# Optimization experiments

Measured on AMD Instinct MI355X. Metric: run time of the kernel, lower is better.

The kernel has to match this reference:

```python
import math
import jax, jax.numpy as jnp
import numpy as np

B, T, E = 2, 2048, 2048
H, HKV = 16, 4
DH = E // H              # 128
ROT_DIM = DH             # rotary_pct = 1.0 -> 128
ROT_HALF = ROT_DIM // 2  # RotaryEmbedding is built with dim=ROT_DIM//2=64; only these dims rotate
MAX_SEQ = 2048


def _rope_tables():
    # theta = 10000 ** (-arange(0, dim, 2)/dim) with dim = ROT_HALF
    theta = 10000.0 ** (-jnp.arange(0, ROT_HALF, 2, dtype=jnp.float32) / ROT_HALF)  # [ROT_HALF//2]
    pos = jnp.arange(MAX_SEQ, dtype=jnp.float32)
    angles = pos[:, None] * theta[None, :]   # [MAX_SEQ, ROT_HALF//2]
    return jnp.cos(angles), jnp.sin(angles)


def _apply_rotary(q, k, start_pos):
    # q: [B,T,H,ROT_DIM], k: [B,T,HKV,ROT_DIM]; rotate only first ROT_HALF dims (interleaved pairs)
    cos, sin = _rope_tables()
    t = q.shape[1]
    cos = jax.lax.dynamic_slice_in_dim(cos, start_pos, t, axis=0)[None, :, None, :]
    sin = jax.lax.dynamic_slice_in_dim(sin, start_pos, t, axis=0)[None, :, None, :]

    def rot(a):
        a_rot, a_pass = a[..., :ROT_HALF], a[..., ROT_HALF:]
        x, y = a_rot[..., 0::2], a_rot[..., 1::2]
        rx = x * cos - y * sin
        ry = x * sin + y * cos
        rotated = jnp.stack([rx, ry], axis=-1).reshape(*a_rot.shape)
        return jnp.concatenate([rotated, a_pass], axis=-1)

    return rot(q), rot(k)


def setup_inputs() -> dict:
    key = jax.random.key(0)
    ks = jax.random.split(key, 9)
    s = 0.02  # weight scale for sane logits
    return {
        "x": jax.random.normal(ks[0], (B, T, E), dtype=jnp.float32),
        "Wq": jax.random.normal(ks[1], (E, H * DH), dtype=jnp.float32) * s,
        "bq": jax.random.normal(ks[2], (H * DH,), dtype=jnp.float32) * s,
        "Wk": jax.random.normal(ks[3], (E, HKV * DH), dtype=jnp.float32) * s,
        "bk": jax.random.normal(ks[4], (HKV * DH,), dtype=jnp.float32) * s,
        "Wv": jax.random.normal(ks[5], (E, HKV * DH), dtype=jnp.float32) * s,
        "bv": jax.random.normal(ks[6], (HKV * DH,), dtype=jnp.float32) * s,
        "Wo": jax.random.normal(ks[7], (E, E), dtype=jnp.float32) * s,
        "bo": jax.random.normal(ks[8], (E,), dtype=jnp.float32) * s,
        "start_pos": 0,
    }


def reference(x, Wq, bq, Wk, bk, Wv, bv, Wo, bo, start_pos):
    b, t, _ = x.shape
    q = (x @ Wq + bq).reshape(b, t, H, DH)
    k = (x @ Wk + bk).reshape(b, t, HKV, DH)
    v = (x @ Wv + bv).reshape(b, t, HKV, DH)

    q, k = _apply_rotary(q, k, start_pos)

    group = H // HKV
    k = jnp.repeat(k, group, axis=2)  # [b,t,H,DH]
    v = jnp.repeat(v, group, axis=2)

    # scores: [b,H,t,t]
    scores = jnp.einsum("bqhd,bkhd->bhqk", q, k) / math.sqrt(DH)
    causal = jnp.tril(jnp.ones((t, t), dtype=bool))
    scores = jnp.where(causal[None, None], scores, -jnp.inf)
    probs = jax.nn.softmax(scores, axis=-1)

    out = jnp.einsum("bhqk,bkhd->bqhd", probs, v).reshape(b, t, H * DH)
    return out @ Wo + bo
```

## Files before the change

kernel.cpp:

```cpp
#include <hip/hip_runtime.h>

typedef __attribute__((ext_vector_type(8))) short short8;
typedef __attribute__((ext_vector_type(4))) float f32x4;
typedef __attribute__((ext_vector_type(16))) float f32x16;

#define DEVFN __device__ __forceinline__

DEVFN unsigned short f2bf(float f) {
  unsigned int u = __builtin_bit_cast(unsigned int, f);
  u += 0x7FFFu + ((u >> 16) & 1u);
  return (unsigned short)(u >> 16);
}
DEVFN float bf2f(unsigned int u) { return __builtin_bit_cast(float, u << 16); }

DEVFN unsigned int cvtpk_bf16(float lo, float hi) {
  unsigned int d;
  asm("v_cvt_pk_bf16_f32 %0, %1, %2" : "=v"(d) : "v"(lo), "v"(hi));
  return d;
}
DEVFN void plswap32(unsigned int& a, unsigned int& b) {
  asm("v_permlane32_swap_b32 %0, %1" : "+v"(a), "+v"(b));
}
DEVFN float bcast32(float v, int srclane) {
  int r = __builtin_amdgcn_ds_bpermute(srclane * 4, __builtin_bit_cast(int, v));
  return __builtin_bit_cast(float, r);
}

__global__ __launch_bounds__(256) void prep_all(
    const float* __restrict__ Wq, const float* __restrict__ Wk, const float* __restrict__ Wv,
    const float* __restrict__ Wo, const float* __restrict__ bq, const float* __restrict__ bk,
    const float* __restrict__ bv, const float* __restrict__ x,
    unsigned short* __restrict__ Wqkvt, unsigned short* __restrict__ Wot,
    unsigned short* __restrict__ xb, float* __restrict__ cost, float* __restrict__ sint,
    float* __restrict__ bcat) {
  __shared__ float lds[32][33];
  const int bid = blockIdx.x, tid = threadIdx.x;
  if (bid < 10240) {
    const float* W; unsigned short* Wt; int ncols, bx, by;
    if (bid < 4096)      { W = Wq; Wt = Wqkvt;                        ncols = 2048; bx = bid & 63; by = bid >> 6; }
    else if (bid < 5120) { int l = bid - 4096; W = Wk; Wt = Wqkvt + (size_t)2048 * 2048; ncols = 512; bx = l & 15; by = l >> 4; }
    else if (bid < 6144) { int l = bid - 5120; W = Wv; Wt = Wqkvt + (size_t)2560 * 2048; ncols = 512; bx = l & 15; by = l >> 4; }
    else                 { int l = bid - 6144; W = Wo; Wt = Wot;      ncols = 2048; bx = l & 63; by = l >> 6; }
    int n0 = bx * 32, k0 = by * 32;
    int tx = tid & 31, ty = tid >> 5;
    #pragma unroll
    for (int i = 0; i < 4; i++) {
      int kr = ty + i * 8;
      lds[kr][tx] = W[(size_t)(k0 + kr) * ncols + n0 + tx];
    }
    __syncthreads();
    #pragma unroll
    for (int i = 0; i < 4; i++) {
      int nr = ty + i * 8;
      Wt[(size_t)(n0 + nr) * 2048 + k0 + tx] = f2bf(lds[tx][nr]);
    }
  } else if (bid < 14336) {
    int gid = (bid - 10240) * 256 + tid;
    const float4* xv = (const float4*)x;
    float4 a = xv[(size_t)gid * 2], b = xv[(size_t)gid * 2 + 1];
    short8 u;
    u[0] = (short)f2bf(a.x); u[1] = (short)f2bf(a.y); u[2] = (short)f2bf(a.z); u[3] = (short)f2bf(a.w);
    u[4] = (short)f2bf(b.x); u[5] = (short)f2bf(b.y); u[6] = (short)f2bf(b.z); u[7] = (short)f2bf(b.w);
    *(short8*)(xb + (size_t)gid * 8) = u;
  } else if (bid < 14592) {
    int gid = (bid - 14336) * 256 + tid;
    int pos = gid >> 5, i = gid & 31;
    float theta = powf(10000.0f, -(float)(2 * i) / 64.0f);
    float ang = (float)pos * theta;
    cost[gid] = cosf(ang);
    sint[gid] = sinf(ang);
  } else {
    int i = (bid - 14592) * 256 + tid;
    float v;
    if (i < 2048) v = bq[i];
    else if (i < 2560) v = bk[i - 2048];
    else v = bv[i - 2560];
    bcat[i] = v;
  }
}

__global__ __launch_bounds__(256) void scatter_all(
    const unsigned short* __restrict__ QKVb, const float* __restrict__ cost,
    const float* __restrict__ sint, const int* __restrict__ spp,
    unsigned short* __restrict__ QFr, unsigned short* __restrict__ KFr,
    unsigned short* __restrict__ VFr) {
  __shared__ __align__(16) unsigned short lds[64 * 128];
  const int bid = blockIdx.x, tid = threadIdx.x;
  if (bid < 20480) {
    int NH, LOG2NH, colOff, gid;
    unsigned short* dst;
    float scale;
    if (bid < 16384) { NH = 16; LOG2NH = 4; colOff = 0;    dst = QFr; scale = 0.12751743f; gid = bid * 256 + tid; }
    else             { NH = 4;  LOG2NH = 2; colOff = 2048; dst = KFr; scale = 1.0f;        gid = (bid - 16384) * 256 + tid; }
    int j = gid & 63;
    int h = (gid >> 6) & (NH - 1);
    int m = gid >> (6 + LOG2NH);
    int t = m & 2047;
    int b = m >> 11;
    const unsigned short* src = QKVb + (size_t)m * 3072 + colOff + h * 128 + 2 * j;
    unsigned int pair = *(const unsigned int*)src;
    float xv = bf2f(pair & 0xFFFFu), yv = bf2f(pair >> 16);
    float rx, ry;
    if (j < 32) {
      int pos = (spp[0] + t) & 2047;
      float c = cost[pos * 32 + j], s = sint[pos * 32 + j];
      rx = xv * c - yv * s;
      ry = xv * s + yv * c;
    } else { rx = xv; ry = yv; }
    rx *= scale; ry *= scale;
    int d0 = 2 * j;
    size_t off = (size_t)(b * NH + h) * 262144 + (t >> 5) * 4096 + (d0 >> 4) * 512
               + ((d0 >> 3) & 1) * 256 + (t & 31) * 8 + (d0 & 7);
    unsigned int outp = (unsigned int)f2bf(rx) | ((unsigned int)f2bf(ry) << 16);
    *(unsigned int*)(dst + off) = outp;
  } else {
    int l = bid - 20480;
    int t0 = (l & 31) * 64;
    int bk = l >> 5;
    const unsigned short* src = QKVb + (size_t)(bk >> 2) * 2048 * 3072 + 2560 + (bk & 3) * 128;
    #pragma unroll
    for (int c = 0; c < 4; c++) {
      int idx = c * 256 + tid;
      int tr = idx >> 4, dc = idx & 15;
      short8 v = *(const short8*)(src + (size_t)(t0 + tr) * 3072 + dc * 8);
      *(short8*)((char*)lds + tr * 256 + 16 * (dc ^ (tr >> 3))) = v;
    }
    __syncthreads();
    unsigned short* dstb = VFr + (size_t)bk * 262144;
    #pragma unroll
    for (int c2 = 0; c2 < 4; c2++) {
      int idx2 = c2 * 256 + tid;
      int tc = idx2 & 7, d = idx2 >> 3;
      short8 u;
      #pragma unroll
      for (int e = 0; e < 8; e++) {
        int t = 8 * tc + e;
        u[e] = *(const short*)((char*)lds + t * 256 + 16 * ((d >> 3) ^ tc) + (d & 7) * 2);
      }
      size_t off = (size_t)(t0 >> 6) * 8192 + ((d >> 5) * 4 + ((tc >> 1) & 3)) * 512
                 + (tc & 1) * 256 + (d & 31) * 8;
      *(short8*)(dstb + off) = u;
    }
  }
}

template<bool BF16OUT>
__global__ __launch_bounds__(512, 1) void gemm256sq(
    const unsigned short* __restrict__ A, const unsigned short* __restrict__ Bt,
    const float* __restrict__ bias, void* __restrict__ Cout, int M, int N, int K, int NTX) {
  __shared__ __align__(16) unsigned short lds[2][32768];
  const int tid = threadIdx.x;
  const int lane = tid & 63, w = tid >> 6;
  const int wrM = w >> 2, wcN = w & 3;
  const int f = blockIdx.x;
  const int cpx = gridDim.x >> 3;
  const int fs = (f & 7) * cpx + (f >> 3);
  const int m0 = (fs / NTX) * 256, n0 = (fs % NTX) * 256;
  const int NT = K >> 6;

  f32x4 acc[8][4];
  #pragma unroll
  for (int i = 0; i < 8; i++)
    #pragma unroll
    for (int j = 0; j < 4; j++)
      #pragma unroll
      for (int r = 0; r < 4; r++) acc[i][j][r] = 0.f;

  const int rr = w * 8 + (lane >> 3);
  const int cc = (lane & 7) ^ (lane >> 3);
  const unsigned short* Asrc = A  + (size_t)(m0 + rr) * K + cc * 8;
  const unsigned short* Bsrc = Bt + (size_t)(n0 + rr) * K + cc * 8;
  const int dstw = w * 512;

  auto STAGE = [&](int b, int kt) {
    unsigned short* bb = &lds[b][0];
    const unsigned short* as = Asrc + kt * 64;
    const unsigned short* bs = Bsrc + kt * 64;
    #pragma unroll
    for (int l = 0; l < 4; l++) {
      __builtin_amdgcn_global_load_lds(
        (const __attribute__((address_space(1))) unsigned int*)(as + (size_t)l * 64 * K),
        (__attribute__((address_space(3))) unsigned int*)(bb + l * 4096 + dstw), 16, 0, 0);
      __builtin_amdgcn_global_load_lds(
        (const __attribute__((address_space(1))) unsigned int*)(bs + (size_t)l * 64 * K),
        (__attribute__((address_space(3))) unsigned int*)(bb + 16384 + l * 4096 + dstw), 16, 0, 0);
    }
  };

  STAGE(0, 0);

  const int lr = lane & 15;
  const int q4 = lane >> 4;
  const int p7 = lane & 7;
  const int so0 = ((q4 ^ p7) * 8);
  const int so1 = (((q4 ^ 4) ^ p7) * 8);
  const int aBase = (wrM * 128 + lr) * 64;
  const int bBase = 16384 + (wcN * 64 + lr) * 64;

  for (int t = 0; t < NT; t++) {
    asm volatile("s_waitcnt vmcnt(0)" ::: "memory");
    __builtin_amdgcn_sched_barrier(0);
    __builtin_amdgcn_s_barrier();
    __builtin_amdgcn_sched_barrier(0);
    if (t + 1 < NT) STAGE((t + 1) & 1, t + 1);
    const unsigned short* bb = &lds[t & 1][0];
    short8 bf0[4], bf1[4];
    #pragma unroll
    for (int ni = 0; ni < 4; ni++) {
      bf0[ni] = *(const short8*)(bb + bBase + ni * 1024 + so0);
      bf1[ni] = *(const short8*)(bb + bBase + ni * 1024 + so1);
    }
    #pragma unroll
    for (int mi = 0; mi < 8; mi++) {
      short8 af0 = *(const short8*)(bb + aBase + mi * 1024 + so0);
      short8 af1 = *(const short8*)(bb + aBase + mi * 1024 + so1);
      __builtin_amdgcn_s_setprio(1);
      #pragma unroll
      for (int ni = 0; ni < 4; ni++) {
        acc[mi][ni] = __builtin_amdgcn_mfma_f32_16x16x32_bf16(af0, bf0[ni], acc[mi][ni], 0, 0, 0);
        acc[mi][ni] = __builtin_amdgcn_mfma_f32_16x16x32_bf16(af1, bf1[ni], acc[mi][ni], 0, 0, 0);
      }
      __builtin_amdgcn_s_setprio(0);
    }
    __builtin_amdgcn_sched_barrier(0);
    __builtin_amdgcn_s_barrier();
  }

  const int cl = lane & 15, rq = lane >> 4;
  #pragma unroll
  for (int mi = 0; mi < 8; mi++) {
    #pragma unroll
    for (int ni = 0; ni < 4; ni++) {
      int gn = n0 + wcN * 64 + ni * 16 + cl;
      float bv = bias[gn];
      #pragma unroll
      for (int r = 0; r < 4; r++) {
        int gm = m0 + wrM * 128 + mi * 16 + rq * 4 + r;
        float v = acc[mi][ni][r] + bv;
        if (BF16OUT) ((unsigned short*)Cout)[(size_t)gm * N + gn] = f2bf(v);
        else ((float*)Cout)[(size_t)gm * N + gn] = v;
      }
    }
  }
}

__global__ __launch_bounds__(256, 2) void attn_kernel(
    const unsigned short* __restrict__ QF, const unsigned short* __restrict__ KF,
    const unsigned short* __restrict__ VF, unsigned short* __restrict__ O) {
  __shared__ __align__(16) unsigned short Kl[2][8192];
  __shared__ __align__(16) unsigned short Vl[2][8192];

  const int tid = threadIdx.x;
  const int lane = tid & 63;
  const int w = tid >> 6;
  const int l31 = lane & 31;
  const int hf = lane >> 5;
  const int bid = blockIdx.x;
  const int g8 = bid & 7;
  const int b = g8 >> 2, kh = g8 & 3;
  const int h = kh * 4 + ((bid >> 3) & 3);
  const int qg = (bid < 256) ? (bid >> 5) : (15 - ((bid - 256) >> 5));
  const int qt = qg * 4 + w;
  const int qw = qt * 32;
  const int ntw = (qt >> 1) + 1;
  const int nbt = 2 * qg + 2;

  const unsigned short* qh  = QF + (size_t)(b * 16 + h) * 262144 + qt * 4096;
  const unsigned short* khp = KF + (size_t)(b * 4 + kh) * 262144;
  const unsigned short* vhp = VF + (size_t)(b * 4 + kh) * 262144;

  short8 qf[8];
  #pragma unroll
  for (int s = 0; s < 8; s++)
    qf[s] = *(const short8*)(qh + s * 512 + lane * 8);

  short8 ones;
  #pragma unroll
  for (int e = 0; e < 8; e++) ones[e] = (short)0x3F80;

  float m_r = -3.0e38f;
  f32x16 oacc[4];
  f32x16 lacc;
  #pragma unroll
  for (int dt = 0; dt < 4; dt++)
    #pragma unroll
    for (int r = 0; r < 16; r++) oacc[dt][r] = 0.f;
  #pragma unroll
  for (int r = 0; r < 16; r++) lacc[r] = 0.f;

  auto STAGE = [&](int buf, int kt) {
    #pragma unroll
    for (int c = 0; c < 4; c++) {
      const int sl = w * 4 + c;
      __builtin_amdgcn_global_load_lds(
        (const __attribute__((address_space(1))) unsigned int*)(khp + (size_t)kt * 8192 + sl * 512 + lane * 8),
        (__attribute__((address_space(3))) unsigned int*)(&Kl[buf][sl * 512]), 16, 0, 0);
      __builtin_amdgcn_global_load_lds(
        (const __attribute__((address_space(1))) unsigned int*)(vhp + (size_t)kt * 8192 + sl * 512 + lane * 8),
        (__attribute__((address_space(3))) unsigned int*)(&Vl[buf][sl * 512]), 16, 0, 0);
    }
  };

  STAGE(0, 0);
  int cur = 0;
  for (int kt = 0; kt < nbt; kt++) {
    __syncthreads();
    if (kt + 1 < nbt) STAGE(cur ^ 1, kt + 1);
    if (kt < ntw) {
      const int kv0 = kt * 64;
      const unsigned short* Kb = &Kl[cur][0];
      const unsigned short* Vb = &Vl[cur][0];
      f32x16 sc[2];
      {
        short8 kf0[8];
        #pragma unroll
        for (int s = 0; s < 8; s++)
          kf0[s] = *(const short8*)(Kb + s * 512 + lane * 8);
        #pragma unroll
        for (int r = 0; r < 16; r++) sc[0][r] = 0.f;
        #pragma unroll
        for (int s = 0; s < 8; s++)
          sc[0] = __builtin_amdgcn_mfma_f32_32x32x16_bf16(kf0[s], qf[s], sc[0], 0, 0, 0);
      }
      {
        short8 kf1[8];
        #pragma unroll
        for (int s = 0; s < 8; s++)
          kf1[s] = *(const short8*)(Kb + (8 + s) * 512 + lane * 8);
        #pragma unroll
        for (int r = 0; r < 16; r++) sc[1][r] = 0.f;
        #pragma unroll
        for (int s = 0; s < 8; s++)
          sc[1] = __builtin_amdgcn_mfma_f32_32x32x16_bf16(kf1[s], qf[s], sc[1], 0, 0, 0);
      }
      short8 vf[4][4];
      #pragma unroll
      for (int dt = 0; dt < 4; dt++)
        #pragma unroll
        for (int ks = 0; ks < 4; ks++)
          vf[dt][ks] = *(const short8*)(Vb + (dt * 4 + ks) * 512 + lane * 8);

      if (kv0 + 63 > qw) {
        #pragma unroll
        for (int ct = 0; ct < 2; ct++)
          #pragma unroll
          for (int r = 0; r < 16; r++) {
            int kg = kv0 + ct * 32 + (r & 3) + 8 * (r >> 2) + 4 * hf;
            if (kg > qw + l31) sc[ct][r] = -3.0e38f;
          }
      }
      float mx[16];
      #pragma unroll
      for (int r = 0; r < 16; r++) mx[r] = fmaxf(sc[0][r], sc[1][r]);
      #pragma unroll
      for (int s2 = 8; s2 >= 1; s2 >>= 1)
        #pragma unroll
        for (int i = 0; i < 8; i++) if (i < s2) mx[i] = fmaxf(mx[i], mx[i + s2]);
      float tm = fmaxf(mx[0], __shfl_xor(mx[0], 32));
      if (__any(tm > m_r + 8.0f)) {
        float mn = fmaxf(m_r, tm);
        float al = __builtin_amdgcn_exp2f(m_r - mn);
        m_r = mn;
        #pragma unroll
        for (int r = 0; r < 16; r++) {
          float alr = bcast32(al, (r & 3) + 8 * (r >> 2) + 4 * hf);
          #pragma unroll
          for (int dt = 0; dt < 4; dt++) oacc[dt][r] *= alr;
          lacc[r] *= alr;
        }
      }
      #pragma unroll
      for (int ct = 0; ct < 2; ct++)
        #pragma unroll
        for (int r = 0; r < 16; r++) sc[ct][r] = __builtin_amdgcn_exp2f(sc[ct][r] - m_r);

      short8 pa[4];
      #pragma unroll
      for (int ks = 0; ks < 4; ks++) {
        const int ct = ks >> 1, kb = (ks & 1) * 8;
        unsigned int A0 = cvtpk_bf16(sc[ct][kb + 0], sc[ct][kb + 1]);
        unsigned int A1 = cvtpk_bf16(sc[ct][kb + 2], sc[ct][kb + 3]);
        unsigned int B0 = cvtpk_bf16(sc[ct][kb + 4], sc[ct][kb + 5]);
        unsigned int B1 = cvtpk_bf16(sc[ct][kb + 6], sc[ct][kb + 7]);
        plswap32(A0, B0);
        plswap32(A1, B1);
        union { unsigned int wds[4]; short8 s8; } u;
        u.wds[0] = A0; u.wds[1] = A1; u.wds[2] = B0; u.wds[3] = B1;
        pa[ks] = u.s8;
      }
      #pragma unroll
      for (int ks = 0; ks < 4; ks++)
        lacc = __builtin_amdgcn_mfma_f32_32x32x16_bf16(pa[ks], ones, lacc, 0, 0, 0);
      #pragma unroll
      for (int dt = 0; dt < 4; dt++)
        #pragma unroll
        for (int ks = 0; ks < 4; ks++)
          oacc[dt] = __builtin_amdgcn_mfma_f32_32x32x16_bf16(pa[ks], vf[dt][ks], oacc[dt], 0, 0, 0);
    }
    cur ^= 1;
  }
  #pragma unroll
  for (int r = 0; r < 16; r++) {
    float inv = 1.0f / lacc[r];
    int rloc = (r & 3) + 8 * (r >> 2) + 4 * hf;
    int qgr = qw + rloc;
    unsigned short* orow = O + ((size_t)(b * 2048 + qgr)) * 2048 + h * 128;
    #pragma unroll
    for (int dt = 0; dt < 4; dt++)
      orow[dt * 32 + l31] = f2bf(oacc[dt][r] * inv);
  }
}

extern "C" void kernel_launch(void* const* d_in, const int* in_sizes, int n_in,
                              void* d_out, int out_size, void* d_ws, size_t ws_size,
                              hipStream_t stream) {
  (void)in_sizes; (void)n_in; (void)out_size; (void)ws_size;
  const float* x  = (const float*)d_in[0];
  const float* Wq = (const float*)d_in[1];
  const float* bq = (const float*)d_in[2];
  const float* Wk = (const float*)d_in[3];
  const float* bk = (const float*)d_in[4];
  const float* Wv = (const float*)d_in[5];
  const float* bv = (const float*)d_in[6];
  const float* Wo = (const float*)d_in[7];
  const float* bo = (const float*)d_in[8];
  const int*   sp = (const int*)d_in[9];

  char* ws = (char*)d_ws;
  unsigned short* xb    = (unsigned short*)ws;
  unsigned short* Wqkvt = (unsigned short*)(ws + 16777216);
  unsigned short* Wot   = (unsigned short*)(ws + 29360128);
  unsigned short* QKVb  = (unsigned short*)(ws + 37748736);
  float* cost           = (float*)(ws + 62914560);
  float* sint           = (float*)(ws + 63176704);
  float* bcat           = (float*)(ws + 63438848);

  unsigned short* Obuf = xb;
  unsigned short* QFr = (unsigned short*)d_out;
  unsigned short* KFr = (unsigned short*)((char*)d_out + 16777216);
  unsigned short* VFr = (unsigned short*)((char*)d_out + 20971520);

  prep_all<<<dim3(14604), 256, 0, stream>>>(Wq, Wk, Wv, Wo, bq, bk, bv, x,
                                            Wqkvt, Wot, xb, cost, sint, bcat);
  gemm256sq<true><<<dim3(192), 512, 0, stream>>>(xb, Wqkvt, bcat, QKVb, 4096, 3072, 2048, 12);
  scatter_all<<<dim3(20736), 256, 0, stream>>>(QKVb, cost, sint, sp, QFr, KFr, VFr);
  attn_kernel<<<dim3(512), 256, 0, stream>>>(QFr, KFr, VFr, Obuf);
  gemm256sq<false><<<dim3(128), 512, 0, stream>>>(Obuf, Wot, bo, (float*)d_out, 4096, 2048, 2048, 8);
}
```

Before: 213.0 us.

## Vectorize RoPE scatter and restructure attention with 8-wave blocks and triple buffering

The Q/K scatter kernel now has each thread handle 8 bf16 elements with 16-byte loads and stores and vectorized cos/sin loads, which cuts the grid size and the per-element indexing overhead. The attention kernel moves to 512-thread blocks in which pairs of waves take complementary causal query tiles (qt and 63-qt) across all four heads of a KV group, so the work is balanced within each block. K/V staging becomes a triple-buffered pipeline with explicit vmcnt waits, which keeps two tiles in flight. The trade-offs are more LDS per block, one block per CU, and hand-tuned waitcnt logic that must stay consistent with the number of outstanding loads.

```diff
diff --git a/kernel.cpp b/kernel.cpp
--- a/kernel.cpp
+++ b/kernel.cpp
@@ -86,35 +86,47 @@
     unsigned short* __restrict__ VFr) {
   __shared__ __align__(16) unsigned short lds[64 * 128];
   const int bid = blockIdx.x, tid = threadIdx.x;
-  if (bid < 20480) {
-    int NH, LOG2NH, colOff, gid;
+  if (bid < 5120) {
+    int NH, colOff, gid, a, h, m;
     unsigned short* dst;
     float scale;
-    if (bid < 16384) { NH = 16; LOG2NH = 4; colOff = 0;    dst = QFr; scale = 0.12751743f; gid = bid * 256 + tid; }
-    else             { NH = 4;  LOG2NH = 2; colOff = 2048; dst = KFr; scale = 1.0f;        gid = (bid - 16384) * 256 + tid; }
-    int j = gid & 63;
-    int h = (gid >> 6) & (NH - 1);
-    int m = gid >> (6 + LOG2NH);
-    int t = m & 2047;
-    int b = m >> 11;
-    const unsigned short* src = QKVb + (size_t)m * 3072 + colOff + h * 128 + 2 * j;
-    unsigned int pair = *(const unsigned int*)src;
-    float xv = bf2f(pair & 0xFFFFu), yv = bf2f(pair >> 16);
-    float rx, ry;
-    if (j < 32) {
+    if (bid < 4096) {
+      NH = 16; colOff = 0; dst = QFr; scale = 0.12751743f;
+      gid = bid * 256 + tid;
+      a = gid & 15; h = (gid >> 4) & 15; m = gid >> 8;
+    } else {
+      NH = 4; colOff = 2048; dst = KFr; scale = 1.0f;
+      gid = (bid - 4096) * 256 + tid;
+      a = gid & 15; h = (gid >> 4) & 3; m = gid >> 6;
+    }
+    int t = m & 2047, b = m >> 11;
+    short8 v = *(const short8*)(QKVb + (size_t)m * 3072 + colOff + h * 128 + 8 * a);
+    float cs[4], sn[4];
+    if (a < 8) {
       int pos = (spp[0] + t) & 2047;
-      float c = cost[pos * 32 + j], s = sint[pos * 32 + j];
-      rx = xv * c - yv * s;
-      ry = xv * s + yv * c;
-    } else { rx = xv; ry = yv; }
-    rx *= scale; ry *= scale;
-    int d0 = 2 * j;
-    size_t off = (size_t)(b * NH + h) * 262144 + (t >> 5) * 4096 + (d0 >> 4) * 512
-               + ((d0 >> 3) & 1) * 256 + (t & 31) * 8 + (d0 & 7);
-    unsigned int outp = (unsigned int)f2bf(rx) | ((unsigned int)f2bf(ry) << 16);
-    *(unsigned int*)(dst + off) = outp;
+      float4 c4 = *(const float4*)(cost + pos * 32 + 4 * a);
+      float4 s4 = *(const float4*)(sint + pos * 32 + 4 * a);
+      cs[0] = c4.x; cs[1] = c4.y; cs[2] = c4.z; cs[3] = c4.w;
+      sn[0] = s4.x; sn[1] = s4.y; sn[2] = s4.z; sn[3] = s4.w;
+    }
+    short8 u;
+    #pragma unroll
+    for (int e = 0; e < 4; e++) {
+      float xv = bf2f((unsigned short)v[2 * e]);
+      float yv = bf2f((unsigned short)v[2 * e + 1]);
+      float rx, ry;
+      if (a < 8) {
+        rx = xv * cs[e] - yv * sn[e];
+        ry = xv * sn[e] + yv * cs[e];
+      } else { rx = xv; ry = yv; }
+      u[2 * e]     = (short)f2bf(rx * scale);
+      u[2 * e + 1] = (short)f2bf(ry * scale);
+    }
+    size_t off = (size_t)(b * NH + h) * 262144 + (t >> 5) * 4096 + (a >> 1) * 512
+               + (a & 1) * 256 + (t & 31) * 8;
+    *(short8*)(dst + off) = u;
   } else {
-    int l = bid - 20480;
+    int l = bid - 5120;
     int t0 = (l & 31) * 64;
     int bk = l >> 5;
     const unsigned short* src = QKVb + (size_t)(bk >> 2) * 2048 * 3072 + 2560 + (bk & 3) * 128;
@@ -244,11 +256,11 @@
   }
 }
 
-__global__ __launch_bounds__(256, 2) void attn_kernel(
+__global__ __launch_bounds__(512, 1) void attn_kernel(
     const unsigned short* __restrict__ QF, const unsigned short* __restrict__ KF,
     const unsigned short* __restrict__ VF, unsigned short* __restrict__ O) {
-  __shared__ __align__(16) unsigned short Kl[2][8192];
-  __shared__ __align__(16) unsigned short Vl[2][8192];
+  __shared__ __align__(16) unsigned short Kl[3][8192];
+  __shared__ __align__(16) unsigned short Vl[3][8192];
 
   const int tid = threadIdx.x;
   const int lane = tid & 63;
@@ -258,12 +270,14 @@
   const int bid = blockIdx.x;
   const int g8 = bid & 7;
   const int b = g8 >> 2, kh = g8 & 3;
-  const int h = kh * 4 + ((bid >> 3) & 3);
-  const int qg = (bid < 256) ? (bid >> 5) : (15 - ((bid - 256) >> 5));
-  const int qt = qg * 4 + w;
+  const int j = bid >> 3;
+  const int hh = w >> 1;
+  const int h = kh * 4 + hh;
+  const int ql = (j + 8 * hh) & 31;
+  const int qt = (w & 1) ? (63 - ql) : ql;
   const int qw = qt * 32;
   const int ntw = (qt >> 1) + 1;
-  const int nbt = 2 * qg + 2;
+  const int nbt = ((63 - (j & 7)) >> 1) + 1;
 
   const unsigned short* qh  = QF + (size_t)(b * 16 + h) * 262144 + qt * 4096;
   const unsigned short* khp = KF + (size_t)(b * 4 + kh) * 262144;
@@ -289,23 +303,29 @@
   for (int r = 0; r < 16; r++) lacc[r] = 0.f;
 
   auto STAGE = [&](int buf, int kt) {
-    #pragma unroll
-    for (int c = 0; c < 4; c++) {
-      const int sl = w * 4 + c;
+    const size_t base = (size_t)kt * 8192;
+    #pragma unroll
+    for (int c = 0; c < 2; c++) {
+      const int sl = w + c * 8;
       __builtin_amdgcn_global_load_lds(
-        (const __attribute__((address_space(1))) unsigned int*)(khp + (size_t)kt * 8192 + sl * 512 + lane * 8),
+        (const __attribute__((address_space(1))) unsigned int*)(khp + base + sl * 512 + lane * 8),
         (__attribute__((address_space(3))) unsigned int*)(&Kl[buf][sl * 512]), 16, 0, 0);
       __builtin_amdgcn_global_load_lds(
-        (const __attribute__((address_space(1))) unsigned int*)(vhp + (size_t)kt * 8192 + sl * 512 + lane * 8),
+        (const __attribute__((address_space(1))) unsigned int*)(vhp + base + sl * 512 + lane * 8),
         (__attribute__((address_space(3))) unsigned int*)(&Vl[buf][sl * 512]), 16, 0, 0);
     }
   };
 
   STAGE(0, 0);
-  int cur = 0;
+  STAGE(1, 1);
   for (int kt = 0; kt < nbt; kt++) {
-    __syncthreads();
-    if (kt + 1 < nbt) STAGE(cur ^ 1, kt + 1);
+    const int cur = kt % 3;
+    if (kt + 1 < nbt) asm volatile("s_waitcnt vmcnt(4)" ::: "memory");
+    else              asm volatile("s_waitcnt vmcnt(0)" ::: "memory");
+    __builtin_amdgcn_sched_barrier(0);
+    __builtin_amdgcn_s_barrier();
+    __builtin_amdgcn_sched_barrier(0);
+    if (kt + 2 < nbt) STAGE((kt + 2) % 3, kt + 2);
     if (kt < ntw) {
       const int kv0 = kt * 64;
       const unsigned short* Kb = &Kl[cur][0];
@@ -397,7 +417,6 @@
         for (int ks = 0; ks < 4; ks++)
           oacc[dt] = __builtin_amdgcn_mfma_f32_32x32x16_bf16(pa[ks], vf[dt][ks], oacc[dt], 0, 0, 0);
     }
-    cur ^= 1;
   }
   #pragma unroll
   for (int r = 0; r < 16; r++) {
@@ -443,7 +462,7 @@
   prep_all<<<dim3(14604), 256, 0, stream>>>(Wq, Wk, Wv, Wo, bq, bk, bv, x,
                                             Wqkvt, Wot, xb, cost, sint, bcat);
   gemm256sq<true><<<dim3(192), 512, 0, stream>>>(xb, Wqkvt, bcat, QKVb, 4096, 3072, 2048, 12);
-  scatter_all<<<dim3(20736), 256, 0, stream>>>(QKVb, cost, sint, sp, QFr, KFr, VFr);
-  attn_kernel<<<dim3(512), 256, 0, stream>>>(QFr, KFr, VFr, Obuf);
+  scatter_all<<<dim3(5376), 256, 0, stream>>>(QKVb, cost, sint, sp, QFr, KFr, VFr);
+  attn_kernel<<<dim3(256), 512, 0, stream>>>(QFr, KFr, VFr, Obuf);
   gemm256sq<false><<<dim3(128), 512, 0, stream>>>(Obuf, Wot, bo, (float*)d_out, 4096, 2048, 2048, 8);
 }
```

New measurement: 220.7 us. +3.6%, slower.
